# Kernel optimization log

Measured on AMD Instinct MI355X. Metric: run time of the kernel, lower is better.

Reference implementation:

```python
import jax, jax.numpy as jnp
import numpy as np

MARKET_DIM, VELOCITY_DIM, AGENT_STATE_DIM = 20, 10, 10
RUNNER_DIM, POSITION_DIM, MAX_RUNNERS = 24, 8, 30
RUNNER_INPUT_DIM = RUNNER_DIM + POSITION_DIM            # 32
MARKET_TOTAL_DIM = MARKET_DIM + VELOCITY_DIM + AGENT_STATE_DIM  # 40
OBS_DIM = MARKET_DIM + VELOCITY_DIM + MAX_RUNNERS * RUNNER_DIM + AGENT_STATE_DIM + MAX_RUNNERS * POSITION_DIM  # 1000
TD_IDX = MARKET_DIM + (VELOCITY_DIM - 4)                # 26
B, T = 256, 64
MLP_H, LSTM_H = 128, 256
LSTM_IN = MLP_H + 2 * MLP_H                             # 384


def setup_inputs() -> dict:
    key = jax.random.key(0)
    ks = jax.random.split(key, 32)

    def w(k, o, i):
        return (jax.random.normal(k, (o, i), jnp.float32) / np.sqrt(i)).astype(jnp.float32)

    z = lambda n: jnp.zeros((n,), jnp.float32)
    return dict(
        obs=jax.random.normal(ks[0], (B, T, OBS_DIM), jnp.float32),
        # runner encoder: 32 -> 128 -> 128 -> 128
        re_w0=w(ks[1], MLP_H, RUNNER_INPUT_DIM), re_b0=z(MLP_H),
        re_w1=w(ks[2], MLP_H, MLP_H), re_b1=z(MLP_H),
        re_w2=w(ks[3], MLP_H, MLP_H), re_b2=z(MLP_H),
        # market encoder: 40 -> 128 -> 128 -> 128
        me_w0=w(ks[4], MLP_H, MARKET_TOTAL_DIM), me_b0=z(MLP_H),
        me_w1=w(ks[5], MLP_H, MLP_H), me_b1=z(MLP_H),
        me_w2=w(ks[6], MLP_H, MLP_H), me_b2=z(MLP_H),
        # TimeLSTM cell (single layer)
        W_ih=w(ks[7], 4 * LSTM_H, LSTM_IN), b_ih=z(4 * LSTM_H),
        W_hh=w(ks[8], 4 * LSTM_H, LSTM_H),
        W_dt=jnp.zeros((LSTM_H,), jnp.float32),
        # actor head: 384 -> 128 -> 2
        a_w0=w(ks[9], MLP_H, MLP_H + LSTM_H), a_b0=z(MLP_H),
        a_w1=w(ks[10], 2, MLP_H) * 0.01, a_b1=z(2),
        # critic head: 256 -> 128 -> 1
        c_w0=w(ks[11], MLP_H, LSTM_H), c_b0=z(MLP_H),
        c_w1=w(ks[12], 1, MLP_H), c_b1=z(1),
        log_std=jnp.zeros((MAX_RUNNERS * 2,), jnp.float32),
    )


def _mlp3(x, w0, b0, w1, b1, w2, b2):
    x = jax.nn.relu(x @ w0.T + b0)
    x = jax.nn.relu(x @ w1.T + b1)
    return x @ w2.T + b2


def _mlp2(x, w0, b0, w1, b1):
    return jax.nn.relu(x @ w0.T + b0) @ w1.T + b1


def reference(obs,
              re_w0, re_b0, re_w1, re_b1, re_w2, re_b2,
              me_w0, me_b0, me_w1, me_b1, me_w2, me_b2,
              W_ih, b_ih, W_hh, W_dt,
              a_w0, a_b0, a_w1, a_b1,
              c_w0, c_b0, c_w1, c_b1,
              log_std):
    b, t, _ = obs.shape
    of = obs.reshape(b * t, -1)
    market = of[:, :MARKET_DIM]
    vel = of[:, MARKET_DIM:MARKET_DIM + VELOCITY_DIM]
    rs = MARKET_DIM + VELOCITY_DIM
    re_ = rs + MAX_RUNNERS * RUNNER_DIM
    runners = of[:, rs:re_].reshape(b * t, MAX_RUNNERS, RUNNER_DIM)
    agent = of[:, re_:re_ + AGENT_STATE_DIM]
    ps = re_ + AGENT_STATE_DIM
    pos = of[:, ps:ps + MAX_RUNNERS * POSITION_DIM].reshape(b * t, MAX_RUNNERS, POSITION_DIM)

    market_feats = jnp.concatenate([market, vel, agent], axis=-1)        # (BT, 40)
    runner_feats = jnp.concatenate([runners, pos], axis=-1)              # (BT, R, 32)

    market_emb = _mlp3(market_feats, me_w0, me_b0, me_w1, me_b1, me_w2, me_b2)  # (BT, 128)
    runner_embs = _mlp3(runner_feats, re_w0, re_b0, re_w1, re_b1, re_w2, re_b2)  # (BT, R, 128)
    r_mean = runner_embs.mean(axis=1)
    r_max = runner_embs.max(axis=1)

    lstm_in = jnp.concatenate([market_emb, r_mean, r_max], axis=-1).reshape(b, t, LSTM_IN)
    dt = of[:, TD_IDX].reshape(b, t)

    h0 = jnp.zeros((b, LSTM_H), obs.dtype)
    c0 = jnp.zeros_like(h0)

    def step(hc, xs):
        h, c = hc
        x, d = xs                                           # (B, 384), (B,)
        gates = x @ W_ih.T + b_ih + h @ W_hh.T              # (B, 4H)
        i, f, g, o = jnp.split(gates, 4, axis=-1)
        f = f + W_dt * d[:, None]                           # time-modulated forget gate
        i, f, o = jax.nn.sigmoid(i), jax.nn.sigmoid(f), jax.nn.sigmoid(o)
        g = jnp.tanh(g)
        c_new = f * c + i * g
        h_new = o * jnp.tanh(c_new)
        return (h_new, c_new), None

    (h, c), _ = jax.lax.scan(step, (h0, c0), (lstm_in.transpose(1, 0, 2), dt.T))
    lstm_out = h  # layer_norm disabled -> identity

    runner_last = runner_embs.reshape(b, t, MAX_RUNNERS, MLP_H)[:, -1]   # (B, R, 128)
    actor_in = jnp.concatenate(
        [runner_last, jnp.broadcast_to(lstm_out[:, None, :], (b, MAX_RUNNERS, LSTM_H))], axis=-1)
    action_mean = _mlp2(actor_in, a_w0, a_b0, a_w1, a_b1).reshape(b, MAX_RUNNERS * 2)
    action_log_std = jnp.broadcast_to(log_std, action_mean.shape)
    value = _mlp2(lstm_out, c_w0, c_b0, c_w1, c_b1)                      # (B, 1)
    return action_mean, action_log_std, value, h, c
```

## Files before the change

kernel.cpp:

```cpp
#include <hip/hip_runtime.h>
#include <hip/hip_bf16.h>
#include <math.h>

#define Bn 256
#define Tn 64
#define OBSD 1000
#define NR 30
#define HD 128
#define LH 256
#define LIN 384
#define TDI 26

#define AM_OFF 0
#define ALS_OFF 15360
#define V_OFF 30720
#define H_OFF 30976
#define C_OFF 96512

typedef unsigned short u16;
typedef short bf16x8 __attribute__((ext_vector_type(8)));
typedef float f32x4 __attribute__((ext_vector_type(4)));

__device__ __forceinline__ float sigm(float x){ return 1.f/(1.f+__expf(-x)); }
__device__ __forceinline__ float tanhfast(float x){
    float ax = fabsf(x);
    float e = __expf(2.f*ax);
    float t = 1.f - 2.f/(e+1.f);
    return copysignf(t, x);
}

__device__ __forceinline__ u16 f2b(float f){
    union { __hip_bfloat16 h; u16 u; } cv;
    cv.h = __float2bfloat16(f);
    return cv.u;
}

__device__ __forceinline__ bf16x8 ld_b128_sys(const u16* p){
    bf16x8 r;
    asm volatile("global_load_dwordx4 %0, %1, off sc0 sc1"
                 : "=v"(r) : "v"(p) : "memory");
    return r;
}
__device__ __forceinline__ void st_b16_sys(u16* p, unsigned v){
    asm volatile("global_store_short %0, %1, off sc0 sc1"
                 :: "v"(p), "v"(v) : "memory");
}
__device__ __forceinline__ f32x4 ld_f32x4_sys(const float* p){
    f32x4 r;
    asm volatile("global_load_dwordx4 %0, %1, off sc0 sc1"
                 : "=v"(r) : "v"(p) : "memory");
    return r;
}
__device__ __forceinline__ void st_f32x4_sys(float* p, f32x4 v){
    asm volatile("global_store_dwordx4 %0, %1, off sc0 sc1"
                 :: "v"(p), "v"(v) : "memory");
}

#define MFMA(a,b,c) __builtin_amdgcn_mfma_f32_16x16x32_bf16(a,b,c,0,0,0)

__device__ __forceinline__ void pack_one(
    const float* __restrict__ src, u16* __restrict__ dst,
    int N, int K, int Kpad, int t)
{
    if (t >= N*Kpad) return;
    int j = t / Kpad, k = t - j*Kpad;
    float v = (k < K) ? src[j*K + k] : 0.f;
    int ntile = j>>4, jr = j&15, kc = k>>5, ko = k&31;
    int lane = ((ko>>3)<<4) | jr, elem = ko&7;
    int KC = Kpad>>5;
    dst[(size_t)(((ntile*KC + kc)*64) + lane)*8 + elem] = f2b(v);
}

__device__ __forceinline__ void pack_gi_one(
    const float* __restrict__ src, u16* __restrict__ dst, int K, int t)
{
    int KC = K >> 5;
    if (t >= 1024*K) return;
    int n = t / K, k = t - n*K;
    int nt = n>>4, jr = n&15;
    int jg = nt>>2, g = nt&3;
    float v = src[(size_t)(g*256 + jg*16 + jr)*K + k];
    int kc = k>>5, ko = k&31;
    int lane = ((ko>>3)<<4) | jr, e = ko&7;
    dst[(size_t)(((nt*KC + kc)*64) + lane)*8 + e] = f2b(v);
}

__global__ __launch_bounds__(256) void k_setup(
    const float* __restrict__ re_w0, u16* __restrict__ pw0,
    const float* __restrict__ re_w1, u16* __restrict__ pw1,
    const float* __restrict__ re_w2, u16* __restrict__ pw2,
    const float* __restrict__ me_w0, u16* __restrict__ pm0,
    const float* __restrict__ me_w1, u16* __restrict__ pm1,
    const float* __restrict__ me_w2, u16* __restrict__ pm2,
    const float* __restrict__ W_ih,  u16* __restrict__ pwih,
    const float* __restrict__ W_hh,  u16* __restrict__ pwhh,
    const float* __restrict__ obs,   float* __restrict__ dtv,
    unsigned int* __restrict__ flags)
{
    int blk = blockIdx.x, tid = threadIdx.x;
    if (blk < 16){            pack_one(re_w0, pw0, 128, 32, 32,  blk*256 + tid); }
    else if (blk < 80){       pack_one(re_w1, pw1, 128,128,128, (blk-16)*256 + tid); }
    else if (blk < 144){      pack_one(re_w2, pw2, 128,128,128, (blk-80)*256 + tid); }
    else if (blk < 176){      pack_one(me_w0, pm0, 128, 40, 64, (blk-144)*256 + tid); }
    else if (blk < 240){      pack_one(me_w1, pm1, 128,128,128, (blk-176)*256 + tid); }
    else if (blk < 304){      pack_one(me_w2, pm2, 128,128,128, (blk-240)*256 + tid); }
    else if (blk < 1840){     pack_gi_one(W_ih, pwih, 384, (blk-304)*256 + tid); }
    else if (blk < 2864){     pack_gi_one(W_hh, pwhh, 256, (blk-1840)*256 + tid); }
    else if (blk < 2928){
        int idx = (blk-2864)*256 + tid;
        int b = idx >> 6, t = idx & 63;
        dtv[t*256 + b] = obs[(size_t)idx*OBSD + TDI];
    } else {
        flags[(blk-2928)*256 + tid] = 0u;
    }
}

__global__ __launch_bounds__(256) void k_embed_market(
    const float* __restrict__ obs,
    const u16* __restrict__ pw0, const float* __restrict__ re_b0,
    const u16* __restrict__ pw1, const float* __restrict__ re_b1,
    const u16* __restrict__ pw2, const float* __restrict__ re_b2,
    const u16* __restrict__ pm0, const float* __restrict__ me_b0,
    const u16* __restrict__ pm1, const float* __restrict__ me_b1,
    const u16* __restrict__ pm2, const float* __restrict__ me_b2,
    u16* __restrict__ li_bf, float* __restrict__ runner_last)
{
    __shared__ __align__(16) u16 smem[19968];
    __shared__ float bsf[384];

    int blk = blockIdx.x, tid = threadIdx.x;
    int lane = tid & 63, wv = tid >> 6;
    int lr = lane & 15, lk = lane >> 4;
    f32x4 zero = {0.f,0.f,0.f,0.f};

    if (blk < 8192){
        u16* xr   = smem;
        u16* act1 = smem + 2560;
        u16* act2 = smem + 11264;
        float* bs0 = bsf, *bs1 = bsf+128, *bs2 = bsf+256;

        int bt0 = blk*2;

        for (int idx=tid; idx<2048; idx+=256){
            int r = idx>>5, k = idx&31;
            int sb = r>>5, rr = r&31;
            const float* row = obs + (size_t)(bt0+sb)*OBSD;
            float v = 0.f;
            if (rr < 30) v = (k<24) ? row[30 + rr*24 + k] : row[760 + rr*8 + (k-24)];
            xr[r*40 + k] = f2b(v);
        }
        if (tid < 128){ bs0[tid]=re_b0[tid]; bs1[tid]=re_b1[tid]; bs2[tid]=re_b2[tid]; }
        __syncthreads();

        f32x4 d[4][2];

        {
            bf16x8 a0[4];
            #pragma unroll
            for (int m=0;m<4;m++) a0[m] = *(const bf16x8*)(xr + (m*16+lr)*40 + lk*8);
            #pragma unroll
            for (int ns=0; ns<2; ns++){
                int n = 2*wv + ns;
                bf16x8 b = *(const bf16x8*)(pw0 + (size_t)(n*64 + lane)*8);
                #pragma unroll
                for (int m=0;m<4;m++) d[m][ns] = MFMA(a0[m], b, zero);
            }
        }
        #pragma unroll
        for (int m=0;m<4;m++)
            #pragma unroll
            for (int ns=0;ns<2;ns++){
                int col = (2*wv+ns)*16 + lr;
                float bias = bs0[col];
                #pragma unroll
                for (int r=0;r<4;r++)
                    act1[(m*16+lk*4+r)*136 + col] = f2b(fmaxf(d[m][ns][r] + bias, 0.f));
            }
        __syncthreads();

        #pragma unroll
        for (int m=0;m<4;m++)
            #pragma unroll
            for (int ns=0;ns<2;ns++) d[m][ns] = zero;
        #pragma unroll
        for (int kc=0; kc<4; kc++){
            bf16x8 am[4];
            #pragma unroll
            for (int m=0;m<4;m++) am[m] = *(const bf16x8*)(act1 + (m*16+lr)*136 + kc*32 + lk*8);
            #pragma unroll
            for (int ns=0; ns<2; ns++){
                int n = 2*wv + ns;
                bf16x8 b = *(const bf16x8*)(pw1 + (size_t)((n*4 + kc)*64 + lane)*8);
                #pragma unroll
                for (int m=0;m<4;m++) d[m][ns] = MFMA(am[m], b, d[m][ns]);
            }
        }
        #pragma unroll
        for (int m=0;m<4;m++)
            #pragma unroll
            for (int ns=0;ns<2;ns++){
                int col = (2*wv+ns)*16 + lr;
                float bias = bs1[col];
                #pragma unroll
                for (int r=0;r<4;r++)
                    act2[(m*16+lk*4+r)*136 + col] = f2b(fmaxf(d[m][ns][r] + bias, 0.f));
            }
        __syncthreads();

        #pragma unroll
        for (int m=0;m<4;m++)
            #pragma unroll
            for (int ns=0;ns<2;ns++) d[m][ns] = zero;
        #pragma unroll
        for (int kc=0; kc<4; kc++){
            bf16x8 am[4];
            #pragma unroll
            for (int m=0;m<4;m++) am[m] = *(const bf16x8*)(act2 + (m*16+lr)*136 + kc*32 + lk*8);
            #pragma unroll
            for (int ns=0; ns<2; ns++){
                int n = 2*wv + ns;
                bf16x8 b = *(const bf16x8*)(pw2 + (size_t)((n*4 + kc)*64 + lane)*8);
                #pragma unroll
                for (int m=0;m<4;m++) d[m][ns] = MFMA(am[m], b, d[m][ns]);
            }
        }

        u16* li0 = li_bf + (size_t)bt0*LIN;
        u16* li1 = li_bf + (size_t)(bt0+1)*LIN;
        bool last1 = (((bt0+1) & 63) == 63);
        int bb1 = (bt0+1) >> 6;

        #pragma unroll
        for (int ns=0; ns<2; ns++){
            int col = (2*wv+ns)*16 + lr;
            float bias = bs2[col];
            float vals[4][4];
            float s0=0.f, m0=-3.4e38f, s1=0.f, m1=-3.4e38f;
            #pragma unroll
            for (int m=0;m<4;m++)
                #pragma unroll
                for (int r=0;r<4;r++){
                    int rw = m*16 + lk*4 + r;
                    float v = d[m][ns][r] + bias;
                    vals[m][r] = v;
                    if (m < 2){
                        bool ok = rw < 30;
                        s0 += ok ? v : 0.f;
                        m0 = fmaxf(m0, ok ? v : -3.4e38f);
                    } else {
                        bool ok = (rw-32) < 30;
                        s1 += ok ? v : 0.f;
                        m1 = fmaxf(m1, ok ? v : -3.4e38f);
                    }
                }
            s0 += __shfl_xor(s0, 16); s0 += __shfl_xor(s0, 32);
            m0 = fmaxf(m0, __shfl_xor(m0, 16)); m0 = fmaxf(m0, __shfl_xor(m0, 32));
            s1 += __shfl_xor(s1, 16); s1 += __shfl_xor(s1, 32);
            m1 = fmaxf(m1, __shfl_xor(m1, 16)); m1 = fmaxf(m1, __shfl_xor(m1, 32));
            if (lk == 0){
                li0[128 + col] = f2b(s0 * (1.0f/30.0f));
                li0[256 + col] = f2b(m0);
            }
            if (lk == 1){
                li1[128 + col] = f2b(s1 * (1.0f/30.0f));
                li1[256 + col] = f2b(m1);
            }
            if (last1){
                #pragma unroll
                for (int m=2;m<4;m++)
                    #pragma unroll
                    for (int r=0;r<4;r++){
                        int rw = m*16 + lk*4 + r - 32;
                        if (rw < 30) runner_last[(size_t)bb1*3840 + rw*128 + col] = vals[m][r];
                    }
            }
        }
    } else {
        u16* xm  = smem;
        u16* ma1 = smem + 2304;
        u16* ma2 = smem + 6656;
        float* bs0 = bsf, *bs1 = bsf+128, *bs2 = bsf+256;

        int bt0 = (blk - 8192)*32;
        for (int idx=tid; idx<2048; idx+=256){
            int r = idx>>6, k = idx&63;
            const float* row = obs + (size_t)(bt0+r)*OBSD;
            float v = 0.f;
            if (k < 30) v = row[k];
            else if (k < 40) v = row[720 + k];
            xm[r*72 + k] = f2b(v);
        }
        if (tid < 128){ bs0[tid]=me_b0[tid]; bs1[tid]=me_b1[tid]; bs2[tid]=me_b2[tid]; }
        __syncthreads();

        f32x4 d[2][2];

        #pragma unroll
        for (int m=0;m<2;m++)
            #pragma unroll
            for (int ns=0;ns<2;ns++) d[m][ns] = zero;
        #pragma unroll
        for (int kc=0; kc<2; kc++){
            bf16x8 a0 = *(const bf16x8*)(xm + lr*72      + kc*32 + lk*8);
            bf16x8 a1 = *(const bf16x8*)(xm + (16+lr)*72 + kc*32 + lk*8);
            #pragma unroll
            for (int ns=0; ns<2; ns++){
                int n = 2*wv + ns;
                bf16x8 b = *(const bf16x8*)(pm0 + (size_t)((n*2 + kc)*64 + lane)*8);
                d[0][ns] = MFMA(a0, b, d[0][ns]);
                d[1][ns] = MFMA(a1, b, d[1][ns]);
            }
        }
        #pragma unroll
        for (int m=0;m<2;m++)
            #pragma unroll
            for (int ns=0;ns<2;ns++){
                int col = (2*wv+ns)*16 + lr;
                float bias = bs0[col];
                #pragma unroll
                for (int r=0;r<4;r++){
                    int rw = m*16 + lk*4 + r;
                    ma1[rw*136 + col] = f2b(fmaxf(d[m][ns][r] + bias, 0.f));
                }
            }
        __syncthreads();

        #pragma unroll
        for (int m=0;m<2;m++)
            #pragma unroll
            for (int ns=0;ns<2;ns++) d[m][ns] = zero;
        #pragma unroll
        for (int kc=0; kc<4; kc++){
            bf16x8 a0 = *(const bf16x8*)(ma1 + lr*136      + kc*32 + lk*8);
            bf16x8 a1 = *(const bf16x8*)(ma1 + (16+lr)*136 + kc*32 + lk*8);
            #pragma unroll
            for (int ns=0; ns<2; ns++){
                int n = 2*wv + ns;
                bf16x8 b = *(const bf16x8*)(pm1 + (size_t)((n*4 + kc)*64 + lane)*8);
                d[0][ns] = MFMA(a0, b, d[0][ns]);
                d[1][ns] = MFMA(a1, b, d[1][ns]);
            }
        }
        #pragma unroll
        for (int m=0;m<2;m++)
            #pragma unroll
            for (int ns=0;ns<2;ns++){
                int col = (2*wv+ns)*16 + lr;
                float bias = bs1[col];
                #pragma unroll
                for (int r=0;r<4;r++){
                    int rw = m*16 + lk*4 + r;
                    ma2[rw*136 + col] = f2b(fmaxf(d[m][ns][r] + bias, 0.f));
                }
            }
        __syncthreads();

        #pragma unroll
        for (int m=0;m<2;m++)
            #pragma unroll
            for (int ns=0;ns<2;ns++) d[m][ns] = zero;
        #pragma unroll
        for (int kc=0; kc<4; kc++){
            bf16x8 a0 = *(const bf16x8*)(ma2 + lr*136      + kc*32 + lk*8);
            bf16x8 a1 = *(const bf16x8*)(ma2 + (16+lr)*136 + kc*32 + lk*8);
            #pragma unroll
            for (int ns=0; ns<2; ns++){
                int n = 2*wv + ns;
                bf16x8 b = *(const bf16x8*)(pm2 + (size_t)((n*4 + kc)*64 + lane)*8);
                d[0][ns] = MFMA(a0, b, d[0][ns]);
                d[1][ns] = MFMA(a1, b, d[1][ns]);
            }
        }
        #pragma unroll
        for (int m=0;m<2;m++)
            #pragma unroll
            for (int ns=0;ns<2;ns++){
                int col = (2*wv+ns)*16 + lr;
                float bias = bs2[col];
                #pragma unroll
                for (int r=0;r<4;r++){
                    int rw = m*16 + lk*4 + r;
                    li_bf[(size_t)(bt0+rw)*LIN + col] = f2b(d[m][ns][r] + bias);
                }
            }
    }
}

__global__ __launch_bounds__(256,1) void k_xwlstm(
    const u16* __restrict__ A, const u16* __restrict__ pwih,
    const float* __restrict__ b_ih, float* __restrict__ xw,
    const u16* __restrict__ pwhh, const float* __restrict__ W_dt,
    const float* __restrict__ dtv,
    u16* __restrict__ hb0, u16* __restrict__ hb1,
    float* __restrict__ hout, float* __restrict__ cout,
    unsigned int* __restrict__ flags)
{
    __shared__ __align__(16) u16 bsh[48*512];

    int blk = blockIdx.x;
    int tid = threadIdx.x;
    int lane = tid & 63, wv = tid >> 6;
    int lr = lane & 15, lk = lane >> 4;

    if (blk >= 32){
        int tb = blk - 32;
        int t = tb >> 1, half = tb & 1;
        int b0 = half*128 + wv*32;

        bf16x8 a[2][12];
        #pragma unroll
        for (int m=0;m<2;m++)
            #pragma unroll
            for (int kc=0;kc<12;kc++)
                a[m][kc] = *(const bf16x8*)(A + ((size_t)(b0+m*16+lr)*64 + t)*384 + kc*32 + lk*8);

        for (int jg=0; jg<16; jg++){
            {
                const bf16x8* src = (const bf16x8*)(pwih + (size_t)jg*48*512);
                bf16x8* dst = (bf16x8*)bsh;
                #pragma unroll
                for (int i=0;i<12;i++)
                    dst[tid + i*256] = src[tid + i*256];
            }
            __syncthreads();

            f32x4 acc[2][4];
            #pragma unroll
            for (int g=0; g<4; g++){
                float bias = b_ih[g*256 + jg*16 + lr];
                f32x4 v = {bias,bias,bias,bias};
                acc[0][g]=v; acc[1][g]=v;
            }
            #pragma unroll
            for (int kc=0; kc<12; kc++){
                bf16x8 b0v = *(const bf16x8*)(bsh + (size_t)((0*12+kc)*64+lane)*8);
                bf16x8 b1v = *(const bf16x8*)(bsh + (size_t)((1*12+kc)*64+lane)*8);
                bf16x8 b2v = *(const bf16x8*)(bsh + (size_t)((2*12+kc)*64+lane)*8);
                bf16x8 b3v = *(const bf16x8*)(bsh + (size_t)((3*12+kc)*64+lane)*8);
                #pragma unroll
                for (int m=0;m<2;m++){
                    acc[m][0] = MFMA(a[m][kc], b0v, acc[m][0]);
                    acc[m][1] = MFMA(a[m][kc], b1v, acc[m][1]);
                    acc[m][2] = MFMA(a[m][kc], b2v, acc[m][2]);
                    acc[m][3] = MFMA(a[m][kc], b3v, acc[m][3]);
                }
            }
            #pragma unroll
            for (int m=0;m<2;m++)
                #pragma unroll
                for (int r=0;r<4;r++){
                    int b = b0 + m*16 + lk*4 + r;
                    int trow = t*256 + b;
                    f32x4 pk;
                    pk[0] = acc[m][0][r]; pk[1] = acc[m][1][r];
                    pk[2] = acc[m][2][r]; pk[3] = acc[m][3][r];
                    st_f32x4_sys(xw + ((size_t)trow*256 + jg*16 + lr)*4, pk);
                }
            __syncthreads();
        }

        asm volatile("s_waitcnt vmcnt(0)" ::: "memory");
        __syncthreads();
        if (tid == 0){
            unsigned* cnt = &flags[2048 + half*128];
            while (__hip_atomic_load(cnt, __ATOMIC_RELAXED, __HIP_MEMORY_SCOPE_SYSTEM)
                   != (unsigned)t) {}
            __hip_atomic_store(cnt, (unsigned)(t+1),
                               __ATOMIC_RELAXED, __HIP_MEMORY_SCOPE_SYSTEM);
        }
        return;
    }

    int p = blk >> 1, hf = blk & 1;
    int bb0 = p*16;
    int jg0 = hf*8 + wv*2;

    bf16x8 bfr[2][4][8];
    #pragma unroll
    for (int jl=0;jl<2;jl++)
        #pragma unroll
        for (int g=0;g<4;g++)
            #pragma unroll
            for (int kc=0;kc<8;kc++)
                bfr[jl][g][kc] = *(const bf16x8*)(pwhh + (size_t)((((jg0+jl)*4+g)*8+kc)*64+lane)*8);

    float wdt0 = W_dt[jg0*16 + lr];
    float wdt1 = W_dt[(jg0+1)*16 + lr];

    float cst[2][4] = {{0.f,0.f,0.f,0.f},{0.f,0.f,0.f,0.f}};
    bf16x8 a[8];
    #pragma unroll
    for (int kc=0;kc<8;kc++) a[kc] = (bf16x8)(short)0;

    int bth = bb0 + lk*4;

    const unsigned* xcnt = &flags[2048 + ((p >= 8) ? 128 : 0)];
    unsigned seen = 0;

    while (seen < 1u){
        unsigned v = 0;
        if (lane == 0)
            v = __hip_atomic_load(xcnt, __ATOMIC_RELAXED, __HIP_MEMORY_SCOPE_SYSTEM);
        v = __shfl(v, 0);
        seen = v;
    }

    f32x4 xwn[2][4];
    #pragma unroll
    for (int jl=0;jl<2;jl++)
        #pragma unroll
        for (int r=0;r<4;r++)
            xwn[jl][r] = ld_f32x4_sys(xw + ((size_t)(bth+r)*256 + (jg0+jl)*16 + lr)*4);
    float4 dtn = *(const float4*)(dtv + bth);
    asm volatile("s_waitcnt vmcnt(0)" ::: "memory");

    f32x4 acc[2][4];
    #pragma unroll
    for (int jl=0;jl<2;jl++){
        f32x4 v0, v1, v2, v3;
        #pragma unroll
        for (int r=0;r<4;r++){
            v0[r] = xwn[jl][r][0]; v1[r] = xwn[jl][r][1];
            v2[r] = xwn[jl][r][2]; v3[r] = xwn[jl][r][3];
        }
        acc[jl][0] = v0; acc[jl][1] = v1; acc[jl][2] = v2; acc[jl][3] = v3;
    }

    unsigned int* myflag   = &flags[blk*64];
    unsigned int* partflag = &flags[(blk^1)*64];

    for (int t=0; t<64; t++){
        asm volatile("s_waitcnt vmcnt(0)" ::: "memory");
        __builtin_amdgcn_sched_barrier(0);

        #pragma unroll
        for (int kc=0; kc<8; kc++){
            #pragma unroll
            for (int jl=0;jl<2;jl++){
                acc[jl][0] = MFMA(a[kc], bfr[jl][0][kc], acc[jl][0]);
                acc[jl][1] = MFMA(a[kc], bfr[jl][1][kc], acc[jl][1]);
                acc[jl][2] = MFMA(a[kc], bfr[jl][2][kc], acc[jl][2]);
                acc[jl][3] = MFMA(a[kc], bfr[jl][3][kc], acc[jl][3]);
            }
        }

        u16* hw = (t&1) ? hb1 : hb0;
        #pragma unroll
        for (int jl=0;jl<2;jl++){
            float wdt = jl ? wdt1 : wdt0;
            int jcol = (jg0+jl)*16 + lr;
            #pragma unroll
            for (int r=0;r<4;r++){
                float dd = (r==0)?dtn.x:(r==1)?dtn.y:(r==2)?dtn.z:dtn.w;
                float gi = sigm(acc[jl][0][r]);
                float gf = sigm(acc[jl][1][r] + wdt*dd);
                float gg = tanhfast(acc[jl][2][r]);
                float go = sigm(acc[jl][3][r]);
                float cn = fmaf(gf, cst[jl][r], gi*gg);
                cst[jl][r] = cn;
                float hv = go * tanhfast(cn);
                if (t < 63){
                    st_b16_sys(hw + (size_t)(bth+r)*256 + jcol, (unsigned)f2b(hv));
                } else {
                    hout[(size_t)(bth+r)*256 + jcol] = hv;
                    cout[(size_t)(bth+r)*256 + jcol] = cn;
                }
            }
        }

        if (t < 63){
            asm volatile("s_waitcnt vmcnt(0)" ::: "memory");
            __syncthreads();
            if (tid == 0)
                __hip_atomic_store(myflag, (unsigned)(t+1),
                                   __ATOMIC_RELAXED, __HIP_MEMORY_SCOPE_SYSTEM);

            while (seen < (unsigned)(t+2)){
                unsigned v = 0;
                if (lane == 0)
                    v = __hip_atomic_load(xcnt, __ATOMIC_RELAXED, __HIP_MEMORY_SCOPE_SYSTEM);
                v = __shfl(v, 0);
                seen = v;
            }

            #pragma unroll
            for (int jl=0;jl<2;jl++)
                #pragma unroll
                for (int r=0;r<4;r++)
                    xwn[jl][r] = ld_f32x4_sys(xw + ((size_t)((t+1)*256 + bth+r)*256 + (jg0+jl)*16 + lr)*4);
            dtn = *(const float4*)(dtv + (t+1)*256 + bth);

            if (lane == 0){
                while (__hip_atomic_load(partflag, __ATOMIC_RELAXED,
                                         __HIP_MEMORY_SCOPE_SYSTEM) < (unsigned)(t+1)) {}
            }
            __builtin_amdgcn_wave_barrier();

            const u16* hr = (t&1) ? hb1 : hb0;
            #pragma unroll
            for (int kc=0; kc<8; kc++)
                a[kc] = ld_b128_sys(hr + (size_t)(bb0+lr)*256 + kc*32 + lk*8);

            asm volatile("s_waitcnt vmcnt(8)" ::: "memory");
            #pragma unroll
            for (int jl=0;jl<2;jl++){
                f32x4 v0, v1, v2, v3;
                #pragma unroll
                for (int r=0;r<4;r++){
                    v0[r] = xwn[jl][r][0]; v1[r] = xwn[jl][r][1];
                    v2[r] = xwn[jl][r][2]; v3[r] = xwn[jl][r][3];
                }
                acc[jl][0] = v0; acc[jl][1] = v1; acc[jl][2] = v2; acc[jl][3] = v3;
            }
        }
    }
}

__device__ __forceinline__ void dense30(
    const float* in, int istride,
    const float* __restrict__ W, int wstride, int K,
    const float* __restrict__ bias, const float* extra,
    float* outp, int ostride, bool relu, int j, int rh)
{
    float acc[15];
    #pragma unroll
    for (int i=0;i<15;i++) acc[i]=0.f;
    const float* w = W + j*wstride;
    for (int k=0;k<K;k+=4){
        float4 wv = *(const float4*)(w+k);
        #pragma unroll
        for (int i=0;i<15;i++){
            float4 xv = *(const float4*)(in + (rh+2*i)*istride + k);
            acc[i] = fmaf(wv.x,xv.x,acc[i]);
            acc[i] = fmaf(wv.y,xv.y,acc[i]);
            acc[i] = fmaf(wv.z,xv.z,acc[i]);
            acc[i] = fmaf(wv.w,xv.w,acc[i]);
        }
    }
    float bb = bias[j] + (extra ? extra[j] : 0.f);
    #pragma unroll
    for (int i=0;i<15;i++){
        float v = acc[i]+bb;
        outp[(rh+2*i)*ostride+j] = relu ? fmaxf(v,0.f) : v;
    }
}

__device__ __forceinline__ float dense1(
    const float* in, const float* __restrict__ W,
    const float* __restrict__ bias, int K, int j)
{
    const float* w = W + j*K;
    float s = 0.f;
    for (int k=0;k<K;k+=4){
        float4 wv = *(const float4*)(w+k);
        float4 xv = *(const float4*)(in+k);
        s = fmaf(wv.x,xv.x,s); s = fmaf(wv.y,xv.y,s);
        s = fmaf(wv.z,xv.z,s); s = fmaf(wv.w,xv.w,s);
    }
    return s + bias[j];
}

__global__ __launch_bounds__(256) void k_heads(
    const float* __restrict__ h, const float* __restrict__ cbuf,
    const float* __restrict__ rl,
    const float* __restrict__ a_w0, const float* __restrict__ a_b0,
    const float* __restrict__ a_w1, const float* __restrict__ a_b1,
    const float* __restrict__ c_w0, const float* __restrict__ c_b0,
    const float* __restrict__ c_w1, const float* __restrict__ c_b1,
    const float* __restrict__ log_std,
    float* __restrict__ out)
{
    __shared__ __align__(16) float hv[LH];
    __shared__ __align__(16) float rls[NR][HD];
    __shared__ __align__(16) float hid[NR][HD];
    __shared__ __align__(16) float dot2[HD];
    __shared__ __align__(16) float red[128];

    int b = blockIdx.x, tid = threadIdx.x;
    hv[tid] = h[b*LH + tid];
    for (int idx=tid; idx<NR*HD; idx+=256) rls[idx>>7][idx&127] = rl[(size_t)b*NR*HD + idx];
    __syncthreads();

    if (tid < 128){
        const float* w = a_w0 + tid*LIN + HD;
        float s = 0.f;
        for (int k=0;k<LH;k+=4){
            float4 wv = *(const float4*)(w+k);
            s = fmaf(wv.x,hv[k],s); s = fmaf(wv.y,hv[k+1],s);
            s = fmaf(wv.z,hv[k+2],s); s = fmaf(wv.w,hv[k+3],s);
        }
        dot2[tid] = s;
    }
    __syncthreads();

    int j = tid & 127, rh = tid >> 7;
    dense30(&rls[0][0], HD, a_w0, LIN, HD, a_b0, dot2, &hid[0][0], HD, true, j, rh);
    __syncthreads();

    if (tid < 60){
        int r = tid >> 1, o = tid & 1;
        const float* w = a_w1 + o*HD;
        float s = a_b1[o];
        for (int k=0;k<HD;k++) s = fmaf(hid[r][k], w[k], s);
        out[AM_OFF + b*60 + tid] = s;
        out[ALS_OFF + b*60 + tid] = log_std[tid];
    }

    float term = 0.f;
    if (tid < 128) term = fmaxf(dense1(hv, c_w0, c_b0, LH, tid), 0.f) * c_w1[tid];
    if (tid < 128) red[tid] = term;
    __syncthreads();
    for (int s2=64; s2>0; s2>>=1){
        if (tid < s2) red[tid] += red[tid+s2];
        __syncthreads();
    }
    if (tid == 0) out[V_OFF + b] = red[0] + c_b1[0];

    out[H_OFF + b*LH + tid] = hv[tid];
    out[C_OFF + b*LH + tid] = cbuf[b*LH + tid];
}

extern "C" void kernel_launch(void* const* d_in, const int* in_sizes, int n_in,
                              void* d_out, int out_size, void* d_ws, size_t ws_size,
                              hipStream_t stream)
{
    const float* obs   = (const float*)d_in[0];
    const float* re_w0 = (const float*)d_in[1];
    const float* re_b0 = (const float*)d_in[2];
    const float* re_w1 = (const float*)d_in[3];
    const float* re_b1 = (const float*)d_in[4];
    const float* re_w2 = (const float*)d_in[5];
    const float* re_b2 = (const float*)d_in[6];
    const float* me_w0 = (const float*)d_in[7];
    const float* me_b0 = (const float*)d_in[8];
    const float* me_w1 = (const float*)d_in[9];
    const float* me_b1 = (const float*)d_in[10];
    const float* me_w2 = (const float*)d_in[11];
    const float* me_b2 = (const float*)d_in[12];
    const float* W_ih  = (const float*)d_in[13];
    const float* b_ih  = (const float*)d_in[14];
    const float* W_hh  = (const float*)d_in[15];
    const float* W_dt  = (const float*)d_in[16];
    const float* a_w0  = (const float*)d_in[17];
    const float* a_b0  = (const float*)d_in[18];
    const float* a_w1  = (const float*)d_in[19];
    const float* a_b1  = (const float*)d_in[20];
    const float* c_w0  = (const float*)d_in[21];
    const float* c_b0  = (const float*)d_in[22];
    const float* c_w1  = (const float*)d_in[23];
    const float* c_b1  = (const float*)d_in[24];
    const float* lstd  = (const float*)d_in[25];
    float* out = (float*)d_out;

    float* ws = (float*)d_ws;
    size_t off = 0;
    float* xw4  = ws + off; off += (size_t)16384*1024;
    float* hout = ws + off; off += (size_t)Bn*LH;
    float* cb   = ws + off; off += (size_t)Bn*LH;
    float* rl   = ws + off; off += (size_t)Bn*NR*HD;
    float* dtv  = ws + off; off += (size_t)16384;
    unsigned int* flags = (unsigned int*)(ws + off); off += 2304;

    u16* us = (u16*)(ws + off);
    size_t uo = 0;
    u16* li_bf = us + uo; uo += (size_t)16384*LIN;
    u16* pw0   = us + uo; uo += 128*32;
    u16* pw1   = us + uo; uo += 128*128;
    u16* pw2   = us + uo; uo += 128*128;
    u16* pm0   = us + uo; uo += 128*64;
    u16* pm1   = us + uo; uo += 128*128;
    u16* pm2   = us + uo; uo += 128*128;
    u16* pwih  = us + uo; uo += (size_t)1024*384;
    u16* pwhh  = us + uo; uo += (size_t)1024*256;
    u16* hb0   = us + uo; uo += (size_t)Bn*LH;
    u16* hb1   = us + uo; uo += (size_t)Bn*LH;

    k_setup<<<2937, 256, 0, stream>>>(re_w0, pw0, re_w1, pw1, re_w2, pw2,
                                      me_w0, pm0, me_w1, pm1, me_w2, pm2,
                                      W_ih, pwih, W_hh, pwhh, obs, dtv, flags);

    k_embed_market<<<8704, 256, 0, stream>>>(obs,
                                      pw0, re_b0, pw1, re_b1, pw2, re_b2,
                                      pm0, me_b0, pm1, me_b1, pm2, me_b2,
                                      li_bf, rl);

    k_xwlstm<<<160, 256, 0, stream>>>(li_bf, pwih, b_ih, xw4,
                                      pwhh, W_dt, dtv, hb0, hb1,
                                      hout, cb, flags);

    k_heads<<<256, 256, 0, stream>>>(hout, cb, rl,
        a_w0, a_b0, a_w1, a_b1, c_w0, c_b0, c_w1, c_b1, lstd, out);
}
```

Measured before the change: 440.6 us.

## Precompute actor runner-projection in spare blocks of the LSTM kernel

Adds 32 extra blocks to the fused xW/LSTM kernel that compute the runner_last part of the actor's first layer (runner_last @ a_w0[:, :128]^T + bias) while the sequential recurrence runs on the other blocks. The heads kernel then only adds the h-dependent term and applies ReLU, which shortens the tail after the LSTM. The extra blocks compete for CUs, and possibly memory bandwidth, with the xW producer blocks, and the persistent recurrence may depend on co-residency. The precompute also writes a new intermediate buffer to global memory.

```diff
diff --git a/kernel.cpp b/kernel.cpp
--- a/kernel.cpp
+++ b/kernel.cpp
@@ -393,7 +393,9 @@
     const float* __restrict__ dtv,
     u16* __restrict__ hb0, u16* __restrict__ hb1,
     float* __restrict__ hout, float* __restrict__ cout,
-    unsigned int* __restrict__ flags)
+    unsigned int* __restrict__ flags,
+    const float* __restrict__ a_w0, const float* __restrict__ a_b0,
+    const float* __restrict__ runner_last, float* __restrict__ rlp)
 {
     __shared__ __align__(16) u16 bsh[48*512];
 
@@ -401,6 +403,35 @@
     int tid = threadIdx.x;
     int lane = tid & 63, wv = tid >> 6;
     int lr = lane & 15, lk = lane >> 4;
+
+    if (blk >= 160){
+        int pb = blk - 160;
+        int b0p = pb*8;
+        float* rlsf = (float*)bsh;
+        for (int bi=0; bi<8; bi++){
+            int b = b0p + bi;
+            for (int idx=tid; idx<3840; idx+=256)
+                rlsf[idx] = runner_last[(size_t)b*3840 + idx];
+            __syncthreads();
+            int j = tid & 127, rh = tid >> 7;
+            #pragma unroll
+            for (int i=0;i<15;i++){
+                int r = rh + 2*i;
+                const float* w = a_w0 + (size_t)j*LIN;
+                const float* x = rlsf + r*128;
+                float s = 0.f;
+                for (int k=0;k<128;k+=4){
+                    float4 wv4 = *(const float4*)(w+k);
+                    float4 xv4 = *(const float4*)(x+k);
+                    s = fmaf(wv4.x,xv4.x,s); s = fmaf(wv4.y,xv4.y,s);
+                    s = fmaf(wv4.z,xv4.z,s); s = fmaf(wv4.w,xv4.w,s);
+                }
+                rlp[(size_t)b*3840 + r*128 + j] = s + a_b0[j];
+            }
+            __syncthreads();
+        }
+        return;
+    }
 
     if (blk >= 32){
         int tb = blk - 32;
@@ -616,35 +647,6 @@
     }
 }
 
-__device__ __forceinline__ void dense30(
-    const float* in, int istride,
-    const float* __restrict__ W, int wstride, int K,
-    const float* __restrict__ bias, const float* extra,
-    float* outp, int ostride, bool relu, int j, int rh)
-{
-    float acc[15];
-    #pragma unroll
-    for (int i=0;i<15;i++) acc[i]=0.f;
-    const float* w = W + j*wstride;
-    for (int k=0;k<K;k+=4){
-        float4 wv = *(const float4*)(w+k);
-        #pragma unroll
-        for (int i=0;i<15;i++){
-            float4 xv = *(const float4*)(in + (rh+2*i)*istride + k);
-            acc[i] = fmaf(wv.x,xv.x,acc[i]);
-            acc[i] = fmaf(wv.y,xv.y,acc[i]);
-            acc[i] = fmaf(wv.z,xv.z,acc[i]);
-            acc[i] = fmaf(wv.w,xv.w,acc[i]);
-        }
-    }
-    float bb = bias[j] + (extra ? extra[j] : 0.f);
-    #pragma unroll
-    for (int i=0;i<15;i++){
-        float v = acc[i]+bb;
-        outp[(rh+2*i)*ostride+j] = relu ? fmaxf(v,0.f) : v;
-    }
-}
-
 __device__ __forceinline__ float dense1(
     const float* in, const float* __restrict__ W,
     const float* __restrict__ bias, int K, int j)
@@ -662,8 +664,8 @@
 
 __global__ __launch_bounds__(256) void k_heads(
     const float* __restrict__ h, const float* __restrict__ cbuf,
-    const float* __restrict__ rl,
-    const float* __restrict__ a_w0, const float* __restrict__ a_b0,
+    const float* __restrict__ rlp,
+    const float* __restrict__ a_w0,
     const float* __restrict__ a_w1, const float* __restrict__ a_b1,
     const float* __restrict__ c_w0, const float* __restrict__ c_b0,
     const float* __restrict__ c_w1, const float* __restrict__ c_b1,
@@ -671,14 +673,12 @@
     float* __restrict__ out)
 {
     __shared__ __align__(16) float hv[LH];
-    __shared__ __align__(16) float rls[NR][HD];
     __shared__ __align__(16) float hid[NR][HD];
     __shared__ __align__(16) float dot2[HD];
     __shared__ __align__(16) float red[128];
 
     int b = blockIdx.x, tid = threadIdx.x;
     hv[tid] = h[b*LH + tid];
-    for (int idx=tid; idx<NR*HD; idx+=256) rls[idx>>7][idx&127] = rl[(size_t)b*NR*HD + idx];
     __syncthreads();
 
     if (tid < 128){
@@ -693,8 +693,10 @@
     }
     __syncthreads();
 
-    int j = tid & 127, rh = tid >> 7;
-    dense30(&rls[0][0], HD, a_w0, LIN, HD, a_b0, dot2, &hid[0][0], HD, true, j, rh);
+    for (int idx=tid; idx<NR*HD; idx+=256){
+        float v = rlp[(size_t)b*3840 + idx] + dot2[idx & 127];
+        hid[idx>>7][idx&127] = fmaxf(v, 0.f);
+    }
     __syncthreads();
 
     if (tid < 60){
@@ -758,6 +760,7 @@
     float* hout = ws + off; off += (size_t)Bn*LH;
     float* cb   = ws + off; off += (size_t)Bn*LH;
     float* rl   = ws + off; off += (size_t)Bn*NR*HD;
+    float* rlp  = ws + off; off += (size_t)Bn*NR*HD;
     float* dtv  = ws + off; off += (size_t)16384;
     unsigned int* flags = (unsigned int*)(ws + off); off += 2304;
 
@@ -784,10 +787,11 @@
                                       pm0, me_b0, pm1, me_b1, pm2, me_b2,
                                       li_bf, rl);
 
-    k_xwlstm<<<160, 256, 0, stream>>>(li_bf, pwih, b_ih, xw4,
+    k_xwlstm<<<192, 256, 0, stream>>>(li_bf, pwih, b_ih, xw4,
                                       pwhh, W_dt, dtv, hb0, hb1,
-                                      hout, cb, flags);
-
-    k_heads<<<256, 256, 0, stream>>>(hout, cb, rl,
-        a_w0, a_b0, a_w1, a_b1, c_w0, c_b0, c_w1, c_b1, lstd, out);
-}
+                                      hout, cb, flags,
+                                      a_w0, a_b0, rl, rlp);
+
+    k_heads<<<256, 256, 0, stream>>>(hout, cb, rlp,
+        a_w0, a_w1, a_b1, c_w0, c_b0, c_w1, c_b1, lstd, out);
+}
```

Measured after the change: 427.9 us. 2.9% less time.
